# Optimization experiments

Hardware: AMD Instinct MI355X
Metric: run time of the kernel (lower is better)

Reference implementation:

```python
import jax, jax.numpy as jnp
import numpy as np

B, L, D, H = 2, 2048, 1024, 16
HD = D // H  # head_dim = 64


def setup_inputs() -> dict:
    key = jax.random.key(0)
    k1, k2, k3, k4, k5 = jax.random.split(key, 5)
    s = 1.0 / np.sqrt(D)
    return {
        "x": jax.random.normal(k1, (B, L, D), dtype=jnp.float32),
        "quantum_scores": jax.random.normal(k2, (B, L, L), dtype=jnp.float32),
        "wq": jax.random.normal(k3, (D, D), dtype=jnp.float32) * s,
        "wk": jax.random.normal(k4, (D, D), dtype=jnp.float32) * s,
        "wv": jax.random.normal(k5, (D, D), dtype=jnp.float32) * s,
        "scale": jnp.ones((H, 1, 1), dtype=jnp.float32),
    }


def reference(x, quantum_scores, wq, wk, wv, scale):
    Bq, Lq, _ = x.shape
    # nn.Linear: y = x @ W^T ; then split heads -> (B, H, L, HD)
    def split_heads(t):
        return t.reshape(Bq, Lq, H, HD).transpose(0, 2, 1, 3)

    q = split_heads(x @ wq.T)
    k = split_heads(x @ wk.T)
    v = split_heads(x @ wv.T)

    logits = jnp.einsum("bhqd,bhkd->bhqk", q, k) / np.sqrt(HD).astype(np.float32)
    logits = logits + quantum_scores[:, None, :, :]          # quantum bias, broadcast over heads
    logits = logits * scale[None, :, :, :]                   # per-head learnable scale
    attn = jax.nn.softmax(logits, axis=-1)
    out = jnp.einsum("bhqk,bhkd->bhqd", attn, v)
    return out.transpose(0, 2, 1, 3).reshape(Bq, Lq, D)
```

## Files before the change

kernel.cpp:

```cpp
#include <hip/hip_runtime.h>

#define Bq 2
#define Lq 2048
#define Dq 1024
#define Hq 16
#define HDq 64

typedef _Float16 f16;
typedef _Float16 f16x8 __attribute__((ext_vector_type(8)));
typedef _Float16 f16x4 __attribute__((ext_vector_type(4)));
typedef __fp16 hf16x2 __attribute__((ext_vector_type(2)));
typedef float f32x4 __attribute__((ext_vector_type(4)));
typedef float f32x16 __attribute__((ext_vector_type(16)));

__device__ __forceinline__ void gload_lds16(const void* g, void* l) {
    __builtin_amdgcn_global_load_lds(
        (const __attribute__((address_space(1))) unsigned int*)g,
        (__attribute__((address_space(3))) unsigned int*)l, 16, 0, 0);
}

__device__ __forceinline__ void swap32(int& a, int& b) {
    asm volatile("v_permlane32_swap_b32 %0, %1" : "+v"(a), "+v"(b));
}

__device__ __forceinline__ int pk2(float a, float b) {
    hf16x2 v = __builtin_amdgcn_cvt_pkrtz(a, b);
    return __builtin_bit_cast(int, v);
}

__global__ __launch_bounds__(256) void convert_kernel(
    const float* __restrict__ x,
    const float* __restrict__ wq, const float* __restrict__ wk, const float* __restrict__ wv,
    f16* __restrict__ x_h, f16* __restrict__ wq_h, f16* __restrict__ wk_h, f16* __restrict__ wv_h)
{
    const int NX = Bq*Lq*Dq;
    const int NW = Dq*Dq;
    const int total4 = (NX + 3*NW) / 4;
    for (int i = blockIdx.x*blockDim.x + threadIdx.x; i < total4;
         i += gridDim.x*blockDim.x) {
        int e = i * 4;
        const float* src; f16* dst; int off;
        if (e < NX) { src = x; dst = x_h; off = e; }
        else {
            int t = e - NX; int w = t >> 20; off = t & (NW-1);
            src = (w==0) ? wq : (w==1) ? wk : wv;
            dst = (w==0) ? wq_h : (w==1) ? wk_h : wv_h;
        }
        float4 v = *reinterpret_cast<const float4*>(src + off);
        f16x4 hv; hv.x=(f16)v.x; hv.y=(f16)v.y; hv.z=(f16)v.z; hv.w=(f16)v.w;
        *reinterpret_cast<f16x4*>(dst + off) = hv;
    }
}

#define GBM 128
#define GBN 128
#define GBK 32

__global__ __launch_bounds__(256) void qkv_qm_fused_kernel(
    const f16* __restrict__ x_h,
    const f16* __restrict__ wq_h, const f16* __restrict__ wk_h, const f16* __restrict__ wv_h,
    const float* __restrict__ quantum,
    f16* __restrict__ q_h, f16* __restrict__ k_h, f16* __restrict__ vT_h,
    f16* __restrict__ qm_pre)
{
    __shared__ __align__(16) char smem[16384];
    const int tid = threadIdx.x;
    const int id  = blockIdx.x;

    if (id < 768) {
        f16* As = (f16*)smem;
        f16* Bs = (f16*)(smem + 8192);
        const int lane = tid & 63;
        const int wave = tid >> 6;
        const int wr = wave >> 1, wc = wave & 1;
        const int l15 = lane & 15, l4 = lane >> 4;
        const int n0 = (id & 7) * GBN;
        const int m0 = ((id >> 3) & 31) * GBM;
        const int z  = id >> 8;
        const f16* W = (z==0) ? wq_h : (z==1) ? wk_h : wv_h;
        const int sslot = tid & 3;

        f32x4 acc[4][4];
        #pragma unroll
        for (int i=0;i<4;++i)
            #pragma unroll
            for (int j=0;j<4;++j) acc[i][j] = f32x4{0.f,0.f,0.f,0.f};

        for (int kt = 0; kt < Dq; kt += GBK) {
            __syncthreads();
            #pragma unroll
            for (int j = 0; j < 2; ++j) {
                int slotIdx = tid + j*256;
                int row = slotIdx >> 2;
                gload_lds16(x_h + (size_t)(m0+row)*Dq + kt + sslot*8,
                            (char*)As + slotIdx*16);
                gload_lds16(W   + (size_t)(n0+row)*Dq + kt + sslot*8,
                            (char*)Bs + slotIdx*16);
            }
            __syncthreads();

            f16x8 a[4], b[4];
            #pragma unroll
            for (int m=0;m<4;++m) {
                int row = wr*64 + m*16 + l15;
                a[m] = *reinterpret_cast<const f16x8*>((const char*)As + row*64 + l4*16);
            }
            #pragma unroll
            for (int n=0;n<4;++n) {
                int row = wc*64 + n*16 + l15;
                b[n] = *reinterpret_cast<const f16x8*>((const char*)Bs + row*64 + l4*16);
            }
            #pragma unroll
            for (int m=0;m<4;++m)
                #pragma unroll
                for (int n=0;n<4;++n)
                    acc[m][n] = __builtin_amdgcn_mfma_f32_16x16x32_f16(a[m], b[n], acc[m][n], 0,0,0);
        }

        #pragma unroll
        for (int m=0;m<4;++m) {
            #pragma unroll
            for (int r=0;r<4;++r) {
                int grow = m0 + wr*64 + m*16 + l4*4 + r;
                int b_   = grow >> 11;
                int lrow = grow & (Lq-1);
                #pragma unroll
                for (int n=0;n<4;++n) {
                    int gcol = n0 + wc*64 + n*16 + l15;
                    int h = gcol >> 6, d = gcol & 63;
                    int bh = b_*Hq + h;
                    f16 val = (f16)acc[m][n][r];
                    if (z==0)      q_h[((size_t)bh*Lq + lrow)*HDq + d] = val;
                    else if (z==1) k_h[((size_t)bh*Lq + lrow)*HDq + d] = val;
                    else           vT_h[((size_t)bh*HDq + d)*Lq + lrow] = val;
                }
            }
        }
    } else {
        float (*qs)[64] = (float(*)[64])smem;
        const int q  = id - 768;
        const int qt = q & 63;
        const int kt = (q >> 6) & 31;
        const int b  = q >> 11;
        const float* base = quantum + ((size_t)b*Lq + qt*32)*Lq + kt*64;
        #pragma unroll
        for (int i=0;i<2;++i) {
            int idx = tid + i*256;
            int r = idx >> 4, c = (idx & 15)*4;
            float4 v = *reinterpret_cast<const float4*>(base + (size_t)r*Lq + c);
            qs[r][c]=v.x; qs[r][c+1]=v.y; qs[r][c+2]=v.z; qs[r][c+3]=v.w;
        }
        __syncthreads();
        const int seg = tid >> 6, lane = tid & 63, l31 = lane & 31, hi = lane >> 5;
        f16x8 u;
        #pragma unroll
        for (int e=0;e<8;++e) {
            int key = 16*seg + 8*(e>>2) + 4*hi + (e&3);
            u[e] = (f16)qs[l31][key];
        }
        f16* outp = qm_pre + (((size_t)b*32 + kt)*64 + qt)*2048 + seg*512 + lane*8;
        *reinterpret_cast<f16x8*>(outp) = u;
    }
}

__global__ __launch_bounds__(256, 2) void attn4_kernel(
    const f16* __restrict__ q_h, const f16* __restrict__ k_h, const f16* __restrict__ vT_h,
    const f16* __restrict__ qm_pre, const float* __restrict__ scale,
    float* __restrict__ out)
{
    __shared__ __align__(16) char lds[65536];

    const int tid  = threadIdx.x;
    const int lane = tid & 63;
    const int wave = tid >> 6;
    const int l31  = lane & 31;
    const int hi   = lane >> 5;
    const int bh = blockIdx.x;
    const int qb = blockIdx.y;
    const int b_ = bh >> 4, h = bh & 15;
    const int qW = qb*128 + wave*32;
    const int qt = qb*4 + wave;
    const float sc = scale[h];
    const float c1 = 0.125f * sc * 1.44269504f;
    const float c2 = sc * 1.44269504f;

    const f16* kbase = k_h  + (size_t)bh*Lq*HDq;
    const f16* vbase = vT_h + (size_t)bh*HDq*Lq;

    f16x8 qf[4];
    {
        const f16* qb_ = q_h + ((size_t)bh*Lq + qW + l31)*HDq + hi*8;
        #pragma unroll
        for (int ds=0; ds<4; ++ds)
            qf[ds] = *reinterpret_cast<const f16x8*>(qb_ + ds*16);
    }

    f32x16 o0, o1;
    #pragma unroll
    for (int r=0;r<16;++r) { o0[r]=0.f; o1[r]=0.f; }
    float m_run = -1e30f, s_run = 0.f;

    auto QTR = [](int t) { return ((t >> 1) & 1)*2 + (t & 1); };

    auto STAGE = [&](int t) {
        const int k0 = t*64;
        char* LK = lds + QTR(t)*16384;
        char* LV = LK + 8192;
        #pragma unroll
        for (int i=0;i<2;++i) {
            int g = tid + i*256;
            int row = g >> 3, slot = g & 7;
            int ss = slot ^ (row & 7);
            gload_lds16(kbase + (size_t)(k0+row)*HDq + ss*8, LK + g*16);
            gload_lds16(vbase + (size_t)row*Lq + k0 + ss*8,  LV + g*16);
        }
    };

    auto QMLOAD = [&](int t, f16x8 (&qm)[4]) {
        const f16* qmb = qm_pre + (((size_t)b_*32 + t)*64 + qt)*2048 + lane*8;
        #pragma unroll
        for (int s=0;s<4;++s)
            qm[s] = *reinterpret_cast<const f16x8*>(qmb + s*512);
    };

    auto COMPUTE = [&](int t, f16x8 (&qmc)[4], f16x8 (&qmn)[4]) {
        const char* LK = lds + QTR(t)*16384;
        const char* LV = LK + 8192;
        int tn = (t+1 < 32) ? t+1 : 31;
        QMLOAD(tn, qmn);

        f32x16 st[2];
        __builtin_amdgcn_s_setprio(1);
        #pragma unroll
        for (int kt=0;kt<2;++kt) {
            #pragma unroll
            for (int r=0;r<16;++r) st[kt][r]=0.f;
            #pragma unroll
            for (int ds=0;ds<4;++ds) {
                f16x8 ka = *reinterpret_cast<const f16x8*>(
                    LK + ((kt*32+l31)<<7) + (((ds*2+hi)^(l31&7))<<4));
                st[kt] = __builtin_amdgcn_mfma_f32_32x32x16_f16(ka, qf[ds], st[kt], 0,0,0);
            }
        }
        __builtin_amdgcn_s_setprio(0);

        float lg[32];
        #pragma unroll
        for (int s=0;s<4;++s)
            #pragma unroll
            for (int e=0;e<8;++e) {
                int i = s*8 + e;
                float sv = (i < 16) ? st[0][i] : st[1][i-16];
                lg[i] = sv*c1 + (float)qmc[s][e]*c2;
            }

        float tm[16];
        #pragma unroll
        for (int r=0;r<16;++r) tm[r] = fmaxf(lg[r], lg[r+16]);
        #pragma unroll
        for (int w=8; w>0; w>>=1)
            #pragma unroll
            for (int r=0;r<w;++r) tm[r] = fmaxf(tm[r], tm[r+w]);
        float tmax = fmaxf(tm[0], __shfl_xor(tm[0], 32));

        if (!__all(tmax <= m_run + 8.f)) {
            float m_new = fmaxf(m_run, tmax);
            float corr = __builtin_amdgcn_exp2f(m_run - m_new);
            m_run = m_new;
            s_run *= corr;
            #pragma unroll
            for (int r=0;r<16;++r) { o0[r] *= corr; o1[r] *= corr; }
        }

        float p[32];
        #pragma unroll
        for (int r=0;r<32;++r) p[r] = __builtin_amdgcn_exp2f(lg[r] - m_run);
        float sm[16];
        #pragma unroll
        for (int r=0;r<16;++r) sm[r] = p[r] + p[r+16];
        #pragma unroll
        for (int w=8; w>0; w>>=1)
            #pragma unroll
            for (int r=0;r<w;++r) sm[r] += sm[r+w];
        s_run += sm[0];

        f16x8 pb[4];
        #pragma unroll
        for (int ks=0; ks<4; ++ks) {
            int w0 = pk2(p[8*ks+0], p[8*ks+1]);
            int w1 = pk2(p[8*ks+2], p[8*ks+3]);
            int w2 = pk2(p[8*ks+4], p[8*ks+5]);
            int w3 = pk2(p[8*ks+6], p[8*ks+7]);
            swap32(w0, w2);
            swap32(w1, w3);
            union { int w[4]; f16x8 v; } u;
            u.w[0]=w0; u.w[1]=w1; u.w[2]=w2; u.w[3]=w3;
            pb[ks] = u.v;
        }

        __builtin_amdgcn_s_setprio(1);
        #pragma unroll
        for (int ks=0; ks<4; ++ks) {
            f16x8 va0 = *reinterpret_cast<const f16x8*>(
                LV + (l31<<7)        + (((ks*2+hi)^(l31&7))<<4));
            f16x8 va1 = *reinterpret_cast<const f16x8*>(
                LV + ((32+l31)<<7)   + (((ks*2+hi)^(l31&7))<<4));
            o0 = __builtin_amdgcn_mfma_f32_32x32x16_f16(va0, pb[ks], o0, 0,0,0);
            o1 = __builtin_amdgcn_mfma_f32_32x32x16_f16(va1, pb[ks], o1, 0,0,0);
        }
        __builtin_amdgcn_s_setprio(0);
    };

    f16x8 qmE[4], qmO[4];

    QMLOAD(0, qmE);
    STAGE(0); STAGE(1);

    #define VMW(n) asm volatile("s_waitcnt vmcnt(" #n ")" ::: "memory")

    VMW(0); __builtin_amdgcn_s_barrier();
    STAGE(2); STAGE(3);
    COMPUTE(0, qmE, qmO);
    COMPUTE(1, qmO, qmE);
    for (int e = 1; e < 15; ++e) {
        VMW(8); __builtin_amdgcn_s_barrier();
        STAGE(2*e+2); STAGE(2*e+3);
        COMPUTE(2*e,   qmE, qmO);
        COMPUTE(2*e+1, qmO, qmE);
    }
    VMW(8); __builtin_amdgcn_s_barrier();
    COMPUTE(30, qmE, qmO);
    COMPUTE(31, qmO, qmE);

    #undef VMW

    float s_tot = s_run + __shfl_xor(s_run, 32);
    float inv = 1.0f / s_tot;
    float* ob = out + ((size_t)b_*Lq + qW + l31)*Dq + h*HDq;
    #pragma unroll
    for (int r=0;r<16;++r) {
        int drow = (r&3) + 8*(r>>2) + 4*hi;
        ob[drow]      = o0[r]*inv;
        ob[32 + drow] = o1[r]*inv;
    }
}

extern "C" void kernel_launch(void* const* d_in, const int* in_sizes, int n_in,
                              void* d_out, int out_size, void* d_ws, size_t ws_size,
                              hipStream_t stream) {
    const float* x       = (const float*)d_in[0];
    const float* quantum = (const float*)d_in[1];
    const float* wq      = (const float*)d_in[2];
    const float* wk      = (const float*)d_in[3];
    const float* wv      = (const float*)d_in[4];
    const float* scale   = (const float*)d_in[5];
    float* out = (float*)d_out;

    f16* ws     = (f16*)d_ws;
    f16* x_h    = ws;
    f16* wq_h   = ws + 4194304;
    f16* wk_h   = ws + 5242880;
    f16* wv_h   = ws + 6291456;
    f16* q_h    = ws + 7340032;
    f16* k_h    = ws + 11534336;
    f16* vT_h   = ws + 15728640;
    f16* qm_pre = ws + 19922944;

    convert_kernel<<<1024, 256, 0, stream>>>(x, wq, wk, wv, x_h, wq_h, wk_h, wv_h);

    qkv_qm_fused_kernel<<<4864, 256, 0, stream>>>(
        x_h, wq_h, wk_h, wv_h, quantum, q_h, k_h, vT_h, qm_pre);

    dim3 g2(Bq*Hq, Lq/128);
    attn4_kernel<<<g2, 256, 0, stream>>>(q_h, k_h, vT_h, qm_pre, scale, out);
}
```

Baseline: 127.1 us.

## Switch attention to 8 waves of 16 queries using 16x16 MFMA tiles

Rewrites the attention kernel to use 512 threads where each wave owns 16 query rows and runs 16x16x32/16x16x16 MFMAs instead of 32x32x16. This removes the permlane swap for P and changes the layout of the precomputed quantum-bias tiles to match. The qm prefetch now happens at the start of each pair of tiles rather than one tile ahead, and each iteration waits on vmcnt(0). That wait drains the next K/V stage before the barrier, which may expose load latency. The aim is higher occupancy and smaller register tiles, at the cost of more per-tile overhead from shuffles and smaller MFMAs.

Result: slower. 131.2 us (+3.2%).

```diff
diff --git a/kernel.cpp b/kernel.cpp
--- a/kernel.cpp
+++ b/kernel.cpp
@@ -11,16 +11,11 @@
 typedef _Float16 f16x4 __attribute__((ext_vector_type(4)));
 typedef __fp16 hf16x2 __attribute__((ext_vector_type(2)));
 typedef float f32x4 __attribute__((ext_vector_type(4)));
-typedef float f32x16 __attribute__((ext_vector_type(16)));
 
 __device__ __forceinline__ void gload_lds16(const void* g, void* l) {
     __builtin_amdgcn_global_load_lds(
         (const __attribute__((address_space(1))) unsigned int*)g,
         (__attribute__((address_space(3))) unsigned int*)l, 16, 0, 0);
-}
-
-__device__ __forceinline__ void swap32(int& a, int& b) {
-    asm volatile("v_permlane32_swap_b32 %0, %1" : "+v"(a), "+v"(b));
 }
 
 __device__ __forceinline__ int pk2(float a, float b) {
@@ -137,12 +132,12 @@
             }
         }
     } else {
-        float (*qs)[64] = (float(*)[64])smem;
+        float (*qs)[65] = (float(*)[65])smem;
         const int q  = id - 768;
-        const int qt = q & 63;
+        const int qt32 = q & 63;
         const int kt = (q >> 6) & 31;
         const int b  = q >> 11;
-        const float* base = quantum + ((size_t)b*Lq + qt*32)*Lq + kt*64;
+        const float* base = quantum + ((size_t)b*Lq + qt32*32)*Lq + kt*64;
         #pragma unroll
         for (int i=0;i<2;++i) {
             int idx = tid + i*256;
@@ -151,19 +146,22 @@
             qs[r][c]=v.x; qs[r][c+1]=v.y; qs[r][c+2]=v.z; qs[r][c+3]=v.w;
         }
         __syncthreads();
-        const int seg = tid >> 6, lane = tid & 63, l31 = lane & 31, hi = lane >> 5;
+        const int seg = tid >> 6;
+        const int half = seg >> 1, frag = seg & 1;
+        const int lane = tid & 63, l15 = lane & 15, l4 = lane >> 4;
         f16x8 u;
         #pragma unroll
         for (int e=0;e<8;++e) {
-            int key = 16*seg + 8*(e>>2) + 4*hi + (e&3);
-            u[e] = (f16)qs[l31][key];
-        }
-        f16* outp = qm_pre + (((size_t)b*32 + kt)*64 + qt)*2048 + seg*512 + lane*8;
+            int key = 16*(frag*2 + (e>>2)) + l4*4 + (e&3);
+            u[e] = (f16)qs[half*16 + l15][key];
+        }
+        f16* outp = qm_pre + (((size_t)b*32 + kt)*128 + qt32*2 + half)*1024
+                    + frag*512 + lane*8;
         *reinterpret_cast<f16x8*>(outp) = u;
     }
 }
 
-__global__ __launch_bounds__(256, 2) void attn4_kernel(
+__global__ __launch_bounds__(512, 4) void attn8_kernel(
     const f16* __restrict__ q_h, const f16* __restrict__ k_h, const f16* __restrict__ vT_h,
     const f16* __restrict__ qm_pre, const float* __restrict__ scale,
     float* __restrict__ out)
@@ -173,13 +171,13 @@
     const int tid  = threadIdx.x;
     const int lane = tid & 63;
     const int wave = tid >> 6;
-    const int l31  = lane & 31;
-    const int hi   = lane >> 5;
+    const int l15  = lane & 15;
+    const int l4   = lane >> 4;
     const int bh = blockIdx.x;
     const int qb = blockIdx.y;
     const int b_ = bh >> 4, h = bh & 15;
-    const int qW = qb*128 + wave*32;
-    const int qt = qb*4 + wave;
+    const int qW = qb*128 + wave*16;
+    const int qt16 = qb*8 + wave;
     const float sc = scale[h];
     const float c1 = 0.125f * sc * 1.44269504f;
     const float c2 = sc * 1.44269504f;
@@ -187,17 +185,16 @@
     const f16* kbase = k_h  + (size_t)bh*Lq*HDq;
     const f16* vbase = vT_h + (size_t)bh*HDq*Lq;
 
-    f16x8 qf[4];
+    f16x8 qf[2];
     {
-        const f16* qb_ = q_h + ((size_t)bh*Lq + qW + l31)*HDq + hi*8;
-        #pragma unroll
-        for (int ds=0; ds<4; ++ds)
-            qf[ds] = *reinterpret_cast<const f16x8*>(qb_ + ds*16);
+        const f16* qb_ = q_h + ((size_t)bh*Lq + qW + l15)*HDq + l4*8;
+        qf[0] = *reinterpret_cast<const f16x8*>(qb_);
+        qf[1] = *reinterpret_cast<const f16x8*>(qb_ + 32);
     }
 
-    f32x16 o0, o1;
+    f32x4 o[4];
     #pragma unroll
-    for (int r=0;r<16;++r) { o0[r]=0.f; o1[r]=0.f; }
+    for (int dt=0;dt<4;++dt) o[dt] = f32x4{0.f,0.f,0.f,0.f};
     float m_run = -1e30f, s_run = 0.f;
 
     auto QTR = [](int t) { return ((t >> 1) & 1)*2 + (t & 1); };
@@ -206,62 +203,56 @@
         const int k0 = t*64;
         char* LK = lds + QTR(t)*16384;
         char* LV = LK + 8192;
-        #pragma unroll
-        for (int i=0;i<2;++i) {
-            int g = tid + i*256;
-            int row = g >> 3, slot = g & 7;
-            int ss = slot ^ (row & 7);
-            gload_lds16(kbase + (size_t)(k0+row)*HDq + ss*8, LK + g*16);
-            gload_lds16(vbase + (size_t)row*Lq + k0 + ss*8,  LV + g*16);
-        }
+        int row = tid >> 3, slot = tid & 7;
+        int ss = slot ^ (row & 7);
+        gload_lds16(kbase + (size_t)(k0+row)*HDq + ss*8, LK + tid*16);
+        gload_lds16(vbase + (size_t)row*Lq + k0 + ss*8,  LV + tid*16);
     };
 
-    auto QMLOAD = [&](int t, f16x8 (&qm)[4]) {
-        const f16* qmb = qm_pre + (((size_t)b_*32 + t)*64 + qt)*2048 + lane*8;
-        #pragma unroll
-        for (int s=0;s<4;++s)
-            qm[s] = *reinterpret_cast<const f16x8*>(qmb + s*512);
+    auto QMLOAD = [&](int t, f16x8 (&qm)[2]) {
+        const f16* qmb = qm_pre + (((size_t)b_*32 + t)*128 + qt16)*1024 + lane*8;
+        qm[0] = *reinterpret_cast<const f16x8*>(qmb);
+        qm[1] = *reinterpret_cast<const f16x8*>(qmb + 512);
     };
 
-    auto COMPUTE = [&](int t, f16x8 (&qmc)[4], f16x8 (&qmn)[4]) {
+    auto TILE = [&](int t, f16x8 (&qm)[2]) {
         const char* LK = lds + QTR(t)*16384;
         const char* LV = LK + 8192;
-        int tn = (t+1 < 32) ? t+1 : 31;
-        QMLOAD(tn, qmn);
-
-        f32x16 st[2];
+
+        f32x4 st[4];
         __builtin_amdgcn_s_setprio(1);
         #pragma unroll
-        for (int kt=0;kt<2;++kt) {
-            #pragma unroll
-            for (int r=0;r<16;++r) st[kt][r]=0.f;
-            #pragma unroll
-            for (int ds=0;ds<4;++ds) {
+        for (int tt=0;tt<4;++tt) {
+            st[tt] = f32x4{0.f,0.f,0.f,0.f};
+            #pragma unroll
+            for (int s=0;s<2;++s) {
+                int krow = tt*16 + l15;
                 f16x8 ka = *reinterpret_cast<const f16x8*>(
-                    LK + ((kt*32+l31)<<7) + (((ds*2+hi)^(l31&7))<<4));
-                st[kt] = __builtin_amdgcn_mfma_f32_32x32x16_f16(ka, qf[ds], st[kt], 0,0,0);
+                    LK + (krow<<7) + (((s*4 + l4) ^ (krow&7))<<4));
+                st[tt] = __builtin_amdgcn_mfma_f32_16x16x32_f16(ka, qf[s], st[tt], 0,0,0);
             }
         }
         __builtin_amdgcn_s_setprio(0);
 
-        float lg[32];
-        #pragma unroll
-        for (int s=0;s<4;++s)
+        float lg[16];
+        #pragma unroll
+        for (int f=0;f<2;++f)
             #pragma unroll
             for (int e=0;e<8;++e) {
-                int i = s*8 + e;
-                float sv = (i < 16) ? st[0][i] : st[1][i-16];
-                lg[i] = sv*c1 + (float)qmc[s][e]*c2;
-            }
-
-        float tm[16];
-        #pragma unroll
-        for (int r=0;r<16;++r) tm[r] = fmaxf(lg[r], lg[r+16]);
-        #pragma unroll
-        for (int w=8; w>0; w>>=1)
+                int tt = f*2 + (e>>2), r = e&3;
+                lg[tt*4+r] = st[tt][r]*c1 + (float)qm[f][e]*c2;
+            }
+
+        float tm[8];
+        #pragma unroll
+        for (int r=0;r<8;++r) tm[r] = fmaxf(lg[r], lg[r+8]);
+        #pragma unroll
+        for (int w=4; w>0; w>>=1)
             #pragma unroll
             for (int r=0;r<w;++r) tm[r] = fmaxf(tm[r], tm[r+w]);
-        float tmax = fmaxf(tm[0], __shfl_xor(tm[0], 32));
+        float tmax = tm[0];
+        tmax = fmaxf(tmax, __shfl_xor(tmax, 16));
+        tmax = fmaxf(tmax, __shfl_xor(tmax, 32));
 
         if (!__all(tmax <= m_run + 8.f)) {
             float m_new = fmaxf(m_run, tmax);
@@ -269,80 +260,66 @@
             m_run = m_new;
             s_run *= corr;
             #pragma unroll
-            for (int r=0;r<16;++r) { o0[r] *= corr; o1[r] *= corr; }
-        }
-
-        float p[32];
-        #pragma unroll
-        for (int r=0;r<32;++r) p[r] = __builtin_amdgcn_exp2f(lg[r] - m_run);
-        float sm[16];
-        #pragma unroll
-        for (int r=0;r<16;++r) sm[r] = p[r] + p[r+16];
-        #pragma unroll
-        for (int w=8; w>0; w>>=1)
+            for (int dt=0;dt<4;++dt) o[dt] *= corr;
+        }
+
+        float p[16];
+        #pragma unroll
+        for (int r=0;r<16;++r) p[r] = __builtin_amdgcn_exp2f(lg[r] - m_run);
+        float sm[8];
+        #pragma unroll
+        for (int r=0;r<8;++r) sm[r] = p[r] + p[r+8];
+        #pragma unroll
+        for (int w=4; w>0; w>>=1)
             #pragma unroll
             for (int r=0;r<w;++r) sm[r] += sm[r+w];
         s_run += sm[0];
 
-        f16x8 pb[4];
-        #pragma unroll
-        for (int ks=0; ks<4; ++ks) {
-            int w0 = pk2(p[8*ks+0], p[8*ks+1]);
-            int w1 = pk2(p[8*ks+2], p[8*ks+3]);
-            int w2 = pk2(p[8*ks+4], p[8*ks+5]);
-            int w3 = pk2(p[8*ks+6], p[8*ks+7]);
-            swap32(w0, w2);
-            swap32(w1, w3);
-            union { int w[4]; f16x8 v; } u;
-            u.w[0]=w0; u.w[1]=w1; u.w[2]=w2; u.w[3]=w3;
-            pb[ks] = u.v;
-        }
-
         __builtin_amdgcn_s_setprio(1);
         #pragma unroll
-        for (int ks=0; ks<4; ++ks) {
-            f16x8 va0 = *reinterpret_cast<const f16x8*>(
-                LV + (l31<<7)        + (((ks*2+hi)^(l31&7))<<4));
-            f16x8 va1 = *reinterpret_cast<const f16x8*>(
-                LV + ((32+l31)<<7)   + (((ks*2+hi)^(l31&7))<<4));
-            o0 = __builtin_amdgcn_mfma_f32_32x32x16_f16(va0, pb[ks], o0, 0,0,0);
-            o1 = __builtin_amdgcn_mfma_f32_32x32x16_f16(va1, pb[ks], o1, 0,0,0);
+        for (int tt=0;tt<4;++tt) {
+            union { int w[2]; f16x4 v; } u;
+            u.w[0] = pk2(p[tt*4+0], p[tt*4+1]);
+            u.w[1] = pk2(p[tt*4+2], p[tt*4+3]);
+            #pragma unroll
+            for (int dt=0;dt<4;++dt) {
+                int d = dt*16 + l15;
+                f16x4 va = *reinterpret_cast<const f16x4*>(
+                    LV + (d<<7) + (((tt*2 + (l4>>1)) ^ (d&7))<<4) + (l4&1)*8);
+                o[dt] = __builtin_amdgcn_mfma_f32_16x16x16f16(va, u.v, o[dt], 0,0,0);
+            }
         }
         __builtin_amdgcn_s_setprio(0);
     };
 
-    f16x8 qmE[4], qmO[4];
-
-    QMLOAD(0, qmE);
+    f16x8 qmA[2], qmB[2];
+
     STAGE(0); STAGE(1);
-
-    #define VMW(n) asm volatile("s_waitcnt vmcnt(" #n ")" ::: "memory")
-
-    VMW(0); __builtin_amdgcn_s_barrier();
-    STAGE(2); STAGE(3);
-    COMPUTE(0, qmE, qmO);
-    COMPUTE(1, qmO, qmE);
-    for (int e = 1; e < 15; ++e) {
-        VMW(8); __builtin_amdgcn_s_barrier();
+    asm volatile("s_waitcnt vmcnt(0)" ::: "memory");
+    __builtin_amdgcn_s_barrier();
+
+    for (int e = 0; e < 15; ++e) {
+        QMLOAD(2*e, qmA); QMLOAD(2*e+1, qmB);
         STAGE(2*e+2); STAGE(2*e+3);
-        COMPUTE(2*e,   qmE, qmO);
-        COMPUTE(2*e+1, qmO, qmE);
+        TILE(2*e,   qmA);
+        TILE(2*e+1, qmB);
+        asm volatile("s_waitcnt vmcnt(0)" ::: "memory");
+        __builtin_amdgcn_s_barrier();
     }
-    VMW(8); __builtin_amdgcn_s_barrier();
-    COMPUTE(30, qmE, qmO);
-    COMPUTE(31, qmO, qmE);
-
-    #undef VMW
-
-    float s_tot = s_run + __shfl_xor(s_run, 32);
+    QMLOAD(30, qmA); QMLOAD(31, qmB);
+    TILE(30, qmA);
+    TILE(31, qmB);
+
+    float s_tot = s_run;
+    s_tot += __shfl_xor(s_tot, 16);
+    s_tot += __shfl_xor(s_tot, 32);
     float inv = 1.0f / s_tot;
-    float* ob = out + ((size_t)b_*Lq + qW + l31)*Dq + h*HDq;
+    float* ob = out + ((size_t)b_*Lq + qW + l15)*Dq + h*HDq;
     #pragma unroll
-    for (int r=0;r<16;++r) {
-        int drow = (r&3) + 8*(r>>2) + 4*hi;
-        ob[drow]      = o0[r]*inv;
-        ob[32 + drow] = o1[r]*inv;
-    }
+    for (int dt=0;dt<4;++dt)
+        #pragma unroll
+        for (int r=0;r<4;++r)
+            ob[dt*16 + l4*4 + r] = o[dt][r]*inv;
 }
 
 extern "C" void kernel_launch(void* const* d_in, const int* in_sizes, int n_in,
@@ -372,5 +349,5 @@
         x_h, wq_h, wk_h, wv_h, quantum, q_h, k_h, vT_h, qm_pre);
 
     dim3 g2(Bq*Hq, Lq/128);
-    attn4_kernel<<<g2, 256, 0, stream>>>(q_h, k_h, vT_h, qm_pre, scale, out);
-}
+    attn8_kernel<<<g2, 512, 0, stream>>>(q_h, k_h, vT_h, qm_pre, scale, out);
+}
```
